# Kernel tuning notes

Measured on AMD Instinct MI355X. Metric: run time of the kernel, lower is better.

## Reference

```python
import jax, jax.numpy as jnp
import numpy as np

N = 4_194_304   # samples per polarization
L = 513         # impulse response taps


def setup_inputs() -> dict:
    key = jax.random.key(0)
    k1, k2, k3, k4 = jax.random.split(key, 4)
    tx_real = jax.random.normal(k1, (2, N), dtype=jnp.float32)
    tx_imag = jax.random.normal(k2, (2, N), dtype=jnp.float32)
    h_real = jax.random.normal(k3, (L,), dtype=jnp.float32)
    h_imag = jax.random.normal(k4, (L,), dtype=jnp.float32)
    return {"tx_real": tx_real, "tx_imag": tx_imag, "h_real": h_real, "h_imag": h_imag}


def reference(tx_real, tx_imag, h_real, h_imag):
    # Dual-pol complex baseband signal [2, N]; same taps h [L] applied to each pol.
    tx = tx_real + 1j * tx_imag          # complex64 [2, N]
    h = h_real + 1j * h_imag             # complex64 [L]
    n_out = tx.shape[-1] + h.shape[0] - 1  # 'full' convolution length
    # FFT-based full convolution, both polarizations batched in one FFT call
    # (mathematically identical to overlap-save convolution in 'full' mode).
    X = jnp.fft.fft(tx, n=n_out, axis=-1)   # [2, n_out]
    H = jnp.fft.fft(h, n=n_out)             # [n_out]
    y = jnp.fft.ifft(X * H[None, :], axis=-1)  # [2, n_out] complex
    # Return real/imag stacked so the output is a real array: [2, n_out, 2]
    return jnp.stack([y.real, y.imag], axis=-1)
```

## Files before the change

### kernel.cpp

```cpp
#include <hip/hip_runtime.h>
#include <hip/hip_bf16.h>


#define NSAMP 4194304
#define LTAPS 513
#define NOUT  (NSAMP + LTAPS - 1)

#define BLK       256
#define WAVE_OUT  1024
#define BLOCK_OUT 4096
#define HALO      512
#define XELEMS    (BLOCK_OUT + HALO + 16)
#define NB        34
#define HROWS     592
#define NBLK      ((NOUT + BLOCK_OUT - 1) / BLOCK_OUT)

typedef __attribute__((ext_vector_type(8)))  short short8;
typedef __attribute__((ext_vector_type(4)))  short short4v;
typedef __attribute__((ext_vector_type(4)))  int   int4v;
typedef __attribute__((ext_vector_type(16))) float float16v;

__device__ __forceinline__ int xswz(int e) { return e ^ (((e >> 6) & 7) << 3); }
#define XSZ 4624

__device__ __forceinline__ short f2b(float f) {
    __bf16 b = (__bf16)f;
    return __builtin_bit_cast(short, b);
}

__global__ __launch_bounds__(BLK)
void build_h(const float* __restrict__ hr, const float* __restrict__ hi,
             short* __restrict__ hh) {
    int R = blockIdx.x * BLK + threadIdx.x;
    if (R < HROWS) {
        short8 vr, vi;
        #pragma unroll
        for (int j = 0; j < 8; ++j) {
            int idx = R - 24 - j;
            bool ok = (idx >= 0) && (idx < LTAPS);
            vr[j] = f2b(ok ? hr[idx] : 0.0f);
            vi[j] = f2b(ok ? hi[idx] : 0.0f);
        }
        *(short8*)(hh + (size_t)(0 * HROWS + R) * 8) = vr;
        *(short8*)(hh + (size_t)(1 * HROWS + R) * 8) = vi;
    }
}

#define MFMA32(A, B, C) __builtin_amdgcn_mfma_f32_32x32x16_bf16((A), (B), (C), 0, 0, 0)

__device__ __forceinline__ short8 bneg8(short8 v) {
    int4v t = __builtin_bit_cast(int4v, v);
    t ^= (int4v){(int)0x80008000, (int)0x80008000, (int)0x80008000, (int)0x80008000};
    return __builtin_bit_cast(short8, t);
}

__global__ __launch_bounds__(BLK, 4)
void fir_mfma32w(const float* __restrict__ txr_all, const float* __restrict__ txi_all,
                 const short* __restrict__ hh, float2* __restrict__ out) {
    const int N0  = blockIdx.x * BLOCK_OUT;
    const int tid = threadIdx.x;

    __shared__ __align__(16) short xs[4][XSZ];

    #pragma unroll
    for (int p = 0; p < 2; ++p) {
        const float* __restrict__ xr_g = txr_all + (size_t)p * NSAMP;
        const float* __restrict__ xi_g = txi_all + (size_t)p * NSAMP;
        #pragma unroll
        for (int it = 0; it < 5; ++it) {
            int e = (tid + it * BLK) * 4;
            if (e < XELEMS) {
                int g = N0 - HALO + e;
                float r0, r1, r2, r3, i0, i1, i2, i3;
                if (g >= 0 && g + 3 < NSAMP) {
                    float4 fr = *(const float4*)(xr_g + g);
                    float4 fi = *(const float4*)(xi_g + g);
                    r0 = fr.x; r1 = fr.y; r2 = fr.z; r3 = fr.w;
                    i0 = fi.x; i1 = fi.y; i2 = fi.z; i3 = fi.w;
                } else {
                    int gc0 = min(max(g + 0, 0), NSAMP - 1);
                    int gc1 = min(max(g + 1, 0), NSAMP - 1);
                    int gc2 = min(max(g + 2, 0), NSAMP - 1);
                    int gc3 = min(max(g + 3, 0), NSAMP - 1);
                    r0 = (g + 0 >= 0 && g + 0 < NSAMP) ? xr_g[gc0] : 0.0f;
                    r1 = (g + 1 >= 0 && g + 1 < NSAMP) ? xr_g[gc1] : 0.0f;
                    r2 = (g + 2 >= 0 && g + 2 < NSAMP) ? xr_g[gc2] : 0.0f;
                    r3 = (g + 3 >= 0 && g + 3 < NSAMP) ? xr_g[gc3] : 0.0f;
                    i0 = (g + 0 >= 0 && g + 0 < NSAMP) ? xi_g[gc0] : 0.0f;
                    i1 = (g + 1 >= 0 && g + 1 < NSAMP) ? xi_g[gc1] : 0.0f;
                    i2 = (g + 2 >= 0 && g + 2 < NSAMP) ? xi_g[gc2] : 0.0f;
                    i3 = (g + 3 >= 0 && g + 3 < NSAMP) ? xi_g[gc3] : 0.0f;
                }
                int ls = xswz(e);
                short4v vr = { f2b(r0), f2b(r1), f2b(r2), f2b(r3) };
                short4v vi = { f2b(i0), f2b(i1), f2b(i2), f2b(i3) };
                *(short4v*)(&xs[2 * p + 0][ls]) = vr;
                *(short4v*)(&xs[2 * p + 1][ls]) = vi;
            }
        }
    }
    __syncthreads();

    const int lane  = tid & 63;
    const int wave  = tid >> 6;
    const int strip = wave;
    const int cc    = lane & 31;
    const int half  = lane >> 5;

    float16v zero = {0.f,0.f,0.f,0.f,0.f,0.f,0.f,0.f,0.f,0.f,0.f,0.f,0.f,0.f,0.f,0.f};
    float16v acc_re0 = zero, acc_im0 = zero, acc_re1 = zero, acc_im1 = zero;

    const int    ebase = HALO + strip * WAVE_OUT + 32 * cc + 8 * half + 16;
    const short* hpr   = hh + (size_t)(cc - 8 * half + 8) * 8;
    const short* xb    = &xs[0][0];

    int ls0 = xswz(ebase);
    short8 fxr0 = *(const short8*)(xb + ls0);
    short8 fxi0 = *(const short8*)(xb + XSZ + ls0);
    short8 fxr1 = *(const short8*)(xb + 2 * XSZ + ls0);
    short8 fxi1 = *(const short8*)(xb + 3 * XSZ + ls0);
    short8 fhr  = *(const short8*)(hpr);
    short8 fhi  = *(const short8*)(hpr + (size_t)HROWS * 8);

    #pragma unroll 2
    for (int b = 0; b < NB; ++b) {
        int en = ebase - 16 * (b + 1);
        en = en < 0 ? 0 : en;
        int lsn = xswz(en);
        short8 nxr0 = *(const short8*)(xb + lsn);
        short8 nxi0 = *(const short8*)(xb + XSZ + lsn);
        short8 nxr1 = *(const short8*)(xb + 2 * XSZ + lsn);
        short8 nxi1 = *(const short8*)(xb + 3 * XSZ + lsn);
        const short* hn = hpr + (size_t)(16 * (b + 1)) * 8;
        short8 nhr = *(const short8*)(hn);
        short8 nhi = *(const short8*)(hn + (size_t)HROWS * 8);

        short8 fnhi = bneg8(fhi);
        acc_re0 = MFMA32(fxr0, fhr,  acc_re0);
        acc_im0 = MFMA32(fxi0, fhr,  acc_im0);
        acc_re1 = MFMA32(fxr1, fhr,  acc_re1);
        acc_im1 = MFMA32(fxi1, fhr,  acc_im1);
        acc_re0 = MFMA32(fxi0, fnhi, acc_re0);
        acc_im0 = MFMA32(fxr0, fhi,  acc_im0);
        acc_re1 = MFMA32(fxi1, fnhi, acc_re1);
        acc_im1 = MFMA32(fxr1, fhi,  acc_im1);

        fxr0 = nxr0; fxi0 = nxi0; fxr1 = nxr1; fxi1 = nxi1;
        fhr  = nhr;  fhi  = nhi;
    }

    float2* __restrict__ op0 = out;
    float2* __restrict__ op1 = out + (size_t)NOUT;
    const int nw = N0 + strip * WAVE_OUT;
    #pragma unroll
    for (int v = 0; v < 16; ++v) {
        int row = (v & 3) + 8 * (v >> 2) + 4 * half;
        int n = nw + 32 * row + cc;
        if (n < NOUT) {
            op0[n] = make_float2(acc_re0[v], acc_im0[v]);
            op1[n] = make_float2(acc_re1[v], acc_im1[v]);
        }
    }
}

extern "C" void kernel_launch(void* const* d_in, const int* in_sizes, int n_in,
                              void* d_out, int out_size, void* d_ws, size_t ws_size,
                              hipStream_t stream) {
    const float* txr = (const float*)d_in[0];
    const float* txi = (const float*)d_in[1];
    const float* hr  = (const float*)d_in[2];
    const float* hi  = (const float*)d_in[3];
    float2* out = (float2*)d_out;
    short* hh = (short*)d_ws;

    build_h<<<dim3((HROWS + BLK - 1) / BLK), BLK, 0, stream>>>(hr, hi, hh);

    fir_mfma32w<<<dim3(NBLK), BLK, 0, stream>>>(txr, txi, hh, out);
}
```

Measured before the change: 140.7 us.

## Persistent double-buffered FIR kernel overlapping next tile loads with MFMA compute

Replaces the one-tile-per-block launch with a persistent grid of 256 blocks of 512 threads. Each block walks 8192-sample tiles, prefetching the next tile's inputs into registers while computing the current tile, then writing them to a second LDS buffer. Taps are copied into LDS once per block. Interior tiles skip the bounds-checked load path, and only edge tiles use it. The cost is higher register and LDS pressure, lower occupancy (2 blocks/CU), and only two tile iterations per block.

Result: no change. 141.8 us (+0.8%).

```diff
diff --git a/kernel.cpp b/kernel.cpp
--- a/kernel.cpp
+++ b/kernel.cpp
@@ -6,14 +6,17 @@
 #define LTAPS 513
 #define NOUT  (NSAMP + LTAPS - 1)
 
-#define BLK       256
+#define BLK       512
 #define WAVE_OUT  1024
-#define BLOCK_OUT 4096
+#define BLOCK_OUT 8192
 #define HALO      512
 #define XELEMS    (BLOCK_OUT + HALO + 16)
 #define NB        34
 #define HROWS     592
-#define NBLK      ((NOUT + BLOCK_OUT - 1) / BLOCK_OUT)
+#define GRID      256
+#define NT        513
+#define XEL_MINI  1552
+#define SITER     5
 
 typedef __attribute__((ext_vector_type(8)))  short short8;
 typedef __attribute__((ext_vector_type(4)))  short short4v;
@@ -21,7 +24,7 @@
 typedef __attribute__((ext_vector_type(16))) float float16v;
 
 __device__ __forceinline__ int xswz(int e) { return e ^ (((e >> 6) & 7) << 3); }
-#define XSZ 4624
+#define XSZ XELEMS
 
 __device__ __forceinline__ short f2b(float f) {
     __bf16 b = (__bf16)f;
@@ -54,112 +57,184 @@
     return __builtin_bit_cast(short8, t);
 }
 
-__global__ __launch_bounds__(BLK, 4)
-void fir_mfma32w(const float* __restrict__ txr_all, const float* __restrict__ txi_all,
-                 const short* __restrict__ hh, float2* __restrict__ out) {
-    const int N0  = blockIdx.x * BLOCK_OUT;
+__device__ __forceinline__ bool tile_edge(int t) { return (t == 0) || (t >= 511); }
+
+__global__ __launch_bounds__(BLK, 2)
+void fir_pipe(const float* __restrict__ txr_all, const float* __restrict__ txi_all,
+              const short* __restrict__ hh, float2* __restrict__ out) {
+    const int bid = blockIdx.x;
     const int tid = threadIdx.x;
 
-    __shared__ __align__(16) short xs[4][XSZ];
-
-    #pragma unroll
-    for (int p = 0; p < 2; ++p) {
-        const float* __restrict__ xr_g = txr_all + (size_t)p * NSAMP;
-        const float* __restrict__ xi_g = txi_all + (size_t)p * NSAMP;
-        #pragma unroll
-        for (int it = 0; it < 5; ++it) {
-            int e = (tid + it * BLK) * 4;
-            if (e < XELEMS) {
-                int g = N0 - HALO + e;
-                float r0, r1, r2, r3, i0, i1, i2, i3;
-                if (g >= 0 && g + 3 < NSAMP) {
-                    float4 fr = *(const float4*)(xr_g + g);
-                    float4 fi = *(const float4*)(xi_g + g);
-                    r0 = fr.x; r1 = fr.y; r2 = fr.z; r3 = fr.w;
-                    i0 = fi.x; i1 = fi.y; i2 = fi.z; i3 = fi.w;
-                } else {
-                    int gc0 = min(max(g + 0, 0), NSAMP - 1);
-                    int gc1 = min(max(g + 1, 0), NSAMP - 1);
-                    int gc2 = min(max(g + 2, 0), NSAMP - 1);
-                    int gc3 = min(max(g + 3, 0), NSAMP - 1);
-                    r0 = (g + 0 >= 0 && g + 0 < NSAMP) ? xr_g[gc0] : 0.0f;
-                    r1 = (g + 1 >= 0 && g + 1 < NSAMP) ? xr_g[gc1] : 0.0f;
-                    r2 = (g + 2 >= 0 && g + 2 < NSAMP) ? xr_g[gc2] : 0.0f;
-                    r3 = (g + 3 >= 0 && g + 3 < NSAMP) ? xr_g[gc3] : 0.0f;
-                    i0 = (g + 0 >= 0 && g + 0 < NSAMP) ? xi_g[gc0] : 0.0f;
-                    i1 = (g + 1 >= 0 && g + 1 < NSAMP) ? xi_g[gc1] : 0.0f;
-                    i2 = (g + 2 >= 0 && g + 2 < NSAMP) ? xi_g[gc2] : 0.0f;
-                    i3 = (g + 3 >= 0 && g + 3 < NSAMP) ? xi_g[gc3] : 0.0f;
+    __shared__ __align__(16) short xs[2][4][XSZ];
+    __shared__ __align__(16) short hl[2 * HROWS * 8];
+
+    {
+        const int4* src = (const int4*)hh;
+        int4* dst = (int4*)hl;
+        #pragma unroll
+        for (int it = 0; it < 3; ++it) {
+            int idx = tid + it * BLK;
+            if (idx < 2 * HROWS) dst[idx] = src[idx];
+        }
+    }
+
+    float4 fr[2][SITER], fi[2][SITER];
+
+    auto stage_load = [&](int t) {
+        if (tile_edge(t)) return;
+        const int N0 = t * BLOCK_OUT;
+        #pragma unroll
+        for (int p = 0; p < 2; ++p) {
+            const float* __restrict__ xr_g = txr_all + (size_t)p * NSAMP + (N0 - HALO);
+            const float* __restrict__ xi_g = txi_all + (size_t)p * NSAMP + (N0 - HALO);
+            #pragma unroll
+            for (int it = 0; it < SITER; ++it) {
+                int e = (tid + it * BLK) * 4;
+                if (e < XELEMS) {
+                    fr[p][it] = *(const float4*)(xr_g + e);
+                    fi[p][it] = *(const float4*)(xi_g + e);
                 }
-                int ls = xswz(e);
-                short4v vr = { f2b(r0), f2b(r1), f2b(r2), f2b(r3) };
-                short4v vi = { f2b(i0), f2b(i1), f2b(i2), f2b(i3) };
-                *(short4v*)(&xs[2 * p + 0][ls]) = vr;
-                *(short4v*)(&xs[2 * p + 1][ls]) = vi;
-            }
-        }
-    }
+            }
+        }
+    };
+
+    auto stage_write = [&](int t, int buf) {
+        if (!tile_edge(t)) {
+            #pragma unroll
+            for (int p = 0; p < 2; ++p) {
+                #pragma unroll
+                for (int it = 0; it < SITER; ++it) {
+                    int e = (tid + it * BLK) * 4;
+                    if (e < XELEMS) {
+                        int ls = xswz(e);
+                        float4 r = fr[p][it], i = fi[p][it];
+                        short4v vr = { f2b(r.x), f2b(r.y), f2b(r.z), f2b(r.w) };
+                        short4v vi = { f2b(i.x), f2b(i.y), f2b(i.z), f2b(i.w) };
+                        *(short4v*)(&xs[buf][2 * p + 0][ls]) = vr;
+                        *(short4v*)(&xs[buf][2 * p + 1][ls]) = vi;
+                    }
+                }
+            }
+        } else {
+            const int N0  = t * BLOCK_OUT;
+            const int xel = (t == NT - 1) ? XEL_MINI : XELEMS;
+            for (int p = 0; p < 2; ++p) {
+                const float* __restrict__ xr_g = txr_all + (size_t)p * NSAMP;
+                const float* __restrict__ xi_g = txi_all + (size_t)p * NSAMP;
+                for (int it = 0; it < SITER; ++it) {
+                    int e = (tid + it * BLK) * 4;
+                    if (e < xel) {
+                        int g = N0 - HALO + e;
+                        float r0, r1, r2, r3, i0, i1, i2, i3;
+                        if (g >= 0 && g + 3 < NSAMP) {
+                            float4 frv = *(const float4*)(xr_g + g);
+                            float4 fiv = *(const float4*)(xi_g + g);
+                            r0 = frv.x; r1 = frv.y; r2 = frv.z; r3 = frv.w;
+                            i0 = fiv.x; i1 = fiv.y; i2 = fiv.z; i3 = fiv.w;
+                        } else {
+                            int gc0 = min(max(g + 0, 0), NSAMP - 1);
+                            int gc1 = min(max(g + 1, 0), NSAMP - 1);
+                            int gc2 = min(max(g + 2, 0), NSAMP - 1);
+                            int gc3 = min(max(g + 3, 0), NSAMP - 1);
+                            r0 = (g + 0 >= 0 && g + 0 < NSAMP) ? xr_g[gc0] : 0.0f;
+                            r1 = (g + 1 >= 0 && g + 1 < NSAMP) ? xr_g[gc1] : 0.0f;
+                            r2 = (g + 2 >= 0 && g + 2 < NSAMP) ? xr_g[gc2] : 0.0f;
+                            r3 = (g + 3 >= 0 && g + 3 < NSAMP) ? xr_g[gc3] : 0.0f;
+                            i0 = (g + 0 >= 0 && g + 0 < NSAMP) ? xi_g[gc0] : 0.0f;
+                            i1 = (g + 1 >= 0 && g + 1 < NSAMP) ? xi_g[gc1] : 0.0f;
+                            i2 = (g + 2 >= 0 && g + 2 < NSAMP) ? xi_g[gc2] : 0.0f;
+                            i3 = (g + 3 >= 0 && g + 3 < NSAMP) ? xi_g[gc3] : 0.0f;
+                        }
+                        int ls = xswz(e);
+                        short4v vr = { f2b(r0), f2b(r1), f2b(r2), f2b(r3) };
+                        short4v vi = { f2b(i0), f2b(i1), f2b(i2), f2b(i3) };
+                        *(short4v*)(&xs[buf][2 * p + 0][ls]) = vr;
+                        *(short4v*)(&xs[buf][2 * p + 1][ls]) = vi;
+                    }
+                }
+            }
+        }
+    };
+
+    const int lane = tid & 63;
+    const int wave = tid >> 6;
+    const int cc   = lane & 31;
+    const int half = lane >> 5;
+    const short* hp0 = hl + (size_t)(cc - 8 * half + 8) * 8;
+
+    auto compute_store = [&](int t, int buf) {
+        const int N0 = t * BLOCK_OUT;
+        const int nw = N0 + wave * WAVE_OUT;
+        if (nw >= NOUT) return;
+
+        float16v zero = {0.f,0.f,0.f,0.f,0.f,0.f,0.f,0.f,0.f,0.f,0.f,0.f,0.f,0.f,0.f,0.f};
+        float16v acc_re0 = zero, acc_im0 = zero, acc_re1 = zero, acc_im1 = zero;
+
+        const int    ebase = HALO + wave * WAVE_OUT + 32 * cc + 8 * half + 16;
+        const short* xb    = &xs[buf][0][0];
+
+        int ls0 = xswz(ebase);
+        short8 fxr0 = *(const short8*)(xb + ls0);
+        short8 fxi0 = *(const short8*)(xb + XSZ + ls0);
+        short8 fxr1 = *(const short8*)(xb + 2 * XSZ + ls0);
+        short8 fxi1 = *(const short8*)(xb + 3 * XSZ + ls0);
+        short8 fhr  = *(const short8*)(hp0);
+        short8 fhi  = *(const short8*)(hp0 + (size_t)HROWS * 8);
+
+        #pragma unroll 2
+        for (int b = 0; b < NB; ++b) {
+            int en = ebase - 16 * (b + 1);
+            en = en < 0 ? 0 : en;
+            int lsn = xswz(en);
+            short8 nxr0 = *(const short8*)(xb + lsn);
+            short8 nxi0 = *(const short8*)(xb + XSZ + lsn);
+            short8 nxr1 = *(const short8*)(xb + 2 * XSZ + lsn);
+            short8 nxi1 = *(const short8*)(xb + 3 * XSZ + lsn);
+            const short* hn = hp0 + (size_t)(16 * (b + 1)) * 8;
+            short8 nhr = *(const short8*)(hn);
+            short8 nhi = *(const short8*)(hn + (size_t)HROWS * 8);
+
+            short8 fnhi = bneg8(fhi);
+            acc_re0 = MFMA32(fxr0, fhr,  acc_re0);
+            acc_im0 = MFMA32(fxi0, fhr,  acc_im0);
+            acc_re1 = MFMA32(fxr1, fhr,  acc_re1);
+            acc_im1 = MFMA32(fxi1, fhr,  acc_im1);
+            acc_re0 = MFMA32(fxi0, fnhi, acc_re0);
+            acc_im0 = MFMA32(fxr0, fhi,  acc_im0);
+            acc_re1 = MFMA32(fxi1, fnhi, acc_re1);
+            acc_im1 = MFMA32(fxr1, fhi,  acc_im1);
+
+            fxr0 = nxr0; fxi0 = nxi0; fxr1 = nxr1; fxi1 = nxi1;
+            fhr  = nhr;  fhi  = nhi;
+        }
+
+        float2* __restrict__ op0 = out;
+        float2* __restrict__ op1 = out + (size_t)NOUT;
+        #pragma unroll
+        for (int v = 0; v < 16; ++v) {
+            int row = (v & 3) + 8 * (v >> 2) + 4 * half;
+            int n = nw + 32 * row + cc;
+            if (n < NOUT) {
+                op0[n] = make_float2(acc_re0[v], acc_im0[v]);
+                op1[n] = make_float2(acc_re1[v], acc_im1[v]);
+            }
+        }
+    };
+
+    stage_load(bid);
+    stage_write(bid, 0);
     __syncthreads();
 
-    const int lane  = tid & 63;
-    const int wave  = tid >> 6;
-    const int strip = wave;
-    const int cc    = lane & 31;
-    const int half  = lane >> 5;
-
-    float16v zero = {0.f,0.f,0.f,0.f,0.f,0.f,0.f,0.f,0.f,0.f,0.f,0.f,0.f,0.f,0.f,0.f};
-    float16v acc_re0 = zero, acc_im0 = zero, acc_re1 = zero, acc_im1 = zero;
-
-    const int    ebase = HALO + strip * WAVE_OUT + 32 * cc + 8 * half + 16;
-    const short* hpr   = hh + (size_t)(cc - 8 * half + 8) * 8;
-    const short* xb    = &xs[0][0];
-
-    int ls0 = xswz(ebase);
-    short8 fxr0 = *(const short8*)(xb + ls0);
-    short8 fxi0 = *(const short8*)(xb + XSZ + ls0);
-    short8 fxr1 = *(const short8*)(xb + 2 * XSZ + ls0);
-    short8 fxi1 = *(const short8*)(xb + 3 * XSZ + ls0);
-    short8 fhr  = *(const short8*)(hpr);
-    short8 fhi  = *(const short8*)(hpr + (size_t)HROWS * 8);
-
-    #pragma unroll 2
-    for (int b = 0; b < NB; ++b) {
-        int en = ebase - 16 * (b + 1);
-        en = en < 0 ? 0 : en;
-        int lsn = xswz(en);
-        short8 nxr0 = *(const short8*)(xb + lsn);
-        short8 nxi0 = *(const short8*)(xb + XSZ + lsn);
-        short8 nxr1 = *(const short8*)(xb + 2 * XSZ + lsn);
-        short8 nxi1 = *(const short8*)(xb + 3 * XSZ + lsn);
-        const short* hn = hpr + (size_t)(16 * (b + 1)) * 8;
-        short8 nhr = *(const short8*)(hn);
-        short8 nhi = *(const short8*)(hn + (size_t)HROWS * 8);
-
-        short8 fnhi = bneg8(fhi);
-        acc_re0 = MFMA32(fxr0, fhr,  acc_re0);
-        acc_im0 = MFMA32(fxi0, fhr,  acc_im0);
-        acc_re1 = MFMA32(fxr1, fhr,  acc_re1);
-        acc_im1 = MFMA32(fxi1, fhr,  acc_im1);
-        acc_re0 = MFMA32(fxi0, fnhi, acc_re0);
-        acc_im0 = MFMA32(fxr0, fhi,  acc_im0);
-        acc_re1 = MFMA32(fxi1, fnhi, acc_re1);
-        acc_im1 = MFMA32(fxr1, fhi,  acc_im1);
-
-        fxr0 = nxr0; fxi0 = nxi0; fxr1 = nxr1; fxi1 = nxi1;
-        fhr  = nhr;  fhi  = nhi;
-    }
-
-    float2* __restrict__ op0 = out;
-    float2* __restrict__ op1 = out + (size_t)NOUT;
-    const int nw = N0 + strip * WAVE_OUT;
-    #pragma unroll
-    for (int v = 0; v < 16; ++v) {
-        int row = (v & 3) + 8 * (v >> 2) + 4 * half;
-        int n = nw + 32 * row + cc;
-        if (n < NOUT) {
-            op0[n] = make_float2(acc_re0[v], acc_im0[v]);
-            op1[n] = make_float2(acc_re1[v], acc_im1[v]);
-        }
+    int cur = 0;
+    for (int t = bid; t < NT; t += GRID) {
+        int tn = t + GRID;
+        if (tn < NT) stage_load(tn);
+        compute_store(t, cur);
+        if (tn < NT) {
+            stage_write(tn, cur ^ 1);
+            __syncthreads();
+        }
+        cur ^= 1;
     }
 }
 
@@ -175,5 +250,5 @@
 
     build_h<<<dim3((HROWS + BLK - 1) / BLK), BLK, 0, stream>>>(hr, hi, hh);
 
-    fir_mfma32w<<<dim3(NBLK), BLK, 0, stream>>>(txr, txi, hh, out);
-}
+    fir_pipe<<<dim3(GRID), BLK, 0, stream>>>(txr, txi, hh, out);
+}
```

## Use fixed 512-block grid with two tiles per block and staggered load/compute phases

Applied to the files above, without the earlier changes.

Replaces the one-tile-per-block launch (1025 blocks) with a fixed grid of 512 blocks, each processing tiles bid and bid+512 using double-buffered LDS. Half of the blocks stage both tiles up front and the other half alternate stage/compute, so memory-bound and MFMA-bound phases are offset across the GPU. A fast path without bounds checks is added for interior tiles, and the last block handles the leftover tile. LDS per block doubles and occupancy bound drops to 2, which can reduce latency hiding.

New measurement: 147.0 us. +4.5%, slower.

```diff
diff --git a/kernel.cpp b/kernel.cpp
--- a/kernel.cpp
+++ b/kernel.cpp
@@ -13,7 +13,9 @@
 #define XELEMS    (BLOCK_OUT + HALO + 16)
 #define NB        34
 #define HROWS     592
-#define NBLK      ((NOUT + BLOCK_OUT - 1) / BLOCK_OUT)
+#define GRID      512
+#define RUNT      1024
+#define SITER     5
 
 typedef __attribute__((ext_vector_type(8)))  short short8;
 typedef __attribute__((ext_vector_type(4)))  short short4v;
@@ -21,7 +23,7 @@
 typedef __attribute__((ext_vector_type(16))) float float16v;
 
 __device__ __forceinline__ int xswz(int e) { return e ^ (((e >> 6) & 7) << 3); }
-#define XSZ 4624
+#define XSZ XELEMS
 
 __device__ __forceinline__ short f2b(float f) {
     __bf16 b = (__bf16)f;
@@ -54,73 +56,97 @@
     return __builtin_bit_cast(short8, t);
 }
 
-__global__ __launch_bounds__(BLK, 4)
-void fir_mfma32w(const float* __restrict__ txr_all, const float* __restrict__ txi_all,
-                 const short* __restrict__ hh, float2* __restrict__ out) {
-    const int N0  = blockIdx.x * BLOCK_OUT;
-    const int tid = threadIdx.x;
-
-    __shared__ __align__(16) short xs[4][XSZ];
-
-    #pragma unroll
-    for (int p = 0; p < 2; ++p) {
-        const float* __restrict__ xr_g = txr_all + (size_t)p * NSAMP;
-        const float* __restrict__ xi_g = txi_all + (size_t)p * NSAMP;
+#define BAR()  do {                                         \
+        asm volatile("s_waitcnt lgkmcnt(0)" ::: "memory");  \
+        __builtin_amdgcn_s_barrier();                       \
+        __builtin_amdgcn_sched_barrier(0);                  \
+    } while (0)
+
+__device__ __forceinline__ void stage_tile(
+        const float* __restrict__ txr_all, const float* __restrict__ txi_all,
+        short (*__restrict__ xsb)[XSZ], int t, int tid) {
+    const int N0 = t * BLOCK_OUT;
+    const bool edge = (t == 0) || (t >= 1023);
+    if (!edge) {
+        const long gb = (long)N0 - HALO;
         #pragma unroll
-        for (int it = 0; it < 5; ++it) {
-            int e = (tid + it * BLK) * 4;
-            if (e < XELEMS) {
-                int g = N0 - HALO + e;
-                float r0, r1, r2, r3, i0, i1, i2, i3;
-                if (g >= 0 && g + 3 < NSAMP) {
-                    float4 fr = *(const float4*)(xr_g + g);
-                    float4 fi = *(const float4*)(xi_g + g);
-                    r0 = fr.x; r1 = fr.y; r2 = fr.z; r3 = fr.w;
-                    i0 = fi.x; i1 = fi.y; i2 = fi.z; i3 = fi.w;
-                } else {
-                    int gc0 = min(max(g + 0, 0), NSAMP - 1);
-                    int gc1 = min(max(g + 1, 0), NSAMP - 1);
-                    int gc2 = min(max(g + 2, 0), NSAMP - 1);
-                    int gc3 = min(max(g + 3, 0), NSAMP - 1);
-                    r0 = (g + 0 >= 0 && g + 0 < NSAMP) ? xr_g[gc0] : 0.0f;
-                    r1 = (g + 1 >= 0 && g + 1 < NSAMP) ? xr_g[gc1] : 0.0f;
-                    r2 = (g + 2 >= 0 && g + 2 < NSAMP) ? xr_g[gc2] : 0.0f;
-                    r3 = (g + 3 >= 0 && g + 3 < NSAMP) ? xr_g[gc3] : 0.0f;
-                    i0 = (g + 0 >= 0 && g + 0 < NSAMP) ? xi_g[gc0] : 0.0f;
-                    i1 = (g + 1 >= 0 && g + 1 < NSAMP) ? xi_g[gc1] : 0.0f;
-                    i2 = (g + 2 >= 0 && g + 2 < NSAMP) ? xi_g[gc2] : 0.0f;
-                    i3 = (g + 3 >= 0 && g + 3 < NSAMP) ? xi_g[gc3] : 0.0f;
+        for (int p = 0; p < 2; ++p) {
+            const float* __restrict__ xr_g = txr_all + (size_t)p * NSAMP + gb;
+            const float* __restrict__ xi_g = txi_all + (size_t)p * NSAMP + gb;
+            #pragma unroll
+            for (int it = 0; it < SITER; ++it) {
+                int e = (tid + it * BLK) * 4;
+                if (e < XELEMS) {
+                    float4 r = *(const float4*)(xr_g + e);
+                    float4 i = *(const float4*)(xi_g + e);
+                    int ls = xswz(e);
+                    short4v vr = { f2b(r.x), f2b(r.y), f2b(r.z), f2b(r.w) };
+                    short4v vi = { f2b(i.x), f2b(i.y), f2b(i.z), f2b(i.w) };
+                    *(short4v*)(&xsb[2 * p + 0][ls]) = vr;
+                    *(short4v*)(&xsb[2 * p + 1][ls]) = vi;
                 }
-                int ls = xswz(e);
-                short4v vr = { f2b(r0), f2b(r1), f2b(r2), f2b(r3) };
-                short4v vi = { f2b(i0), f2b(i1), f2b(i2), f2b(i3) };
-                *(short4v*)(&xs[2 * p + 0][ls]) = vr;
-                *(short4v*)(&xs[2 * p + 1][ls]) = vi;
             }
         }
-    }
-    __syncthreads();
-
-    const int lane  = tid & 63;
-    const int wave  = tid >> 6;
-    const int strip = wave;
-    const int cc    = lane & 31;
-    const int half  = lane >> 5;
+    } else {
+        for (int p = 0; p < 2; ++p) {
+            const float* __restrict__ xr_g = txr_all + (size_t)p * NSAMP;
+            const float* __restrict__ xi_g = txi_all + (size_t)p * NSAMP;
+            for (int it = 0; it < SITER; ++it) {
+                int e = (tid + it * BLK) * 4;
+                if (e < XELEMS) {
+                    int g = N0 - HALO + e;
+                    float r0, r1, r2, r3, i0, i1, i2, i3;
+                    if (g >= 0 && g + 3 < NSAMP) {
+                        float4 fr = *(const float4*)(xr_g + g);
+                        float4 fi = *(const float4*)(xi_g + g);
+                        r0 = fr.x; r1 = fr.y; r2 = fr.z; r3 = fr.w;
+                        i0 = fi.x; i1 = fi.y; i2 = fi.z; i3 = fi.w;
+                    } else {
+                        int gc0 = min(max(g + 0, 0), NSAMP - 1);
+                        int gc1 = min(max(g + 1, 0), NSAMP - 1);
+                        int gc2 = min(max(g + 2, 0), NSAMP - 1);
+                        int gc3 = min(max(g + 3, 0), NSAMP - 1);
+                        r0 = (g + 0 >= 0 && g + 0 < NSAMP) ? xr_g[gc0] : 0.0f;
+                        r1 = (g + 1 >= 0 && g + 1 < NSAMP) ? xr_g[gc1] : 0.0f;
+                        r2 = (g + 2 >= 0 && g + 2 < NSAMP) ? xr_g[gc2] : 0.0f;
+                        r3 = (g + 3 >= 0 && g + 3 < NSAMP) ? xr_g[gc3] : 0.0f;
+                        i0 = (g + 0 >= 0 && g + 0 < NSAMP) ? xi_g[gc0] : 0.0f;
+                        i1 = (g + 1 >= 0 && g + 1 < NSAMP) ? xi_g[gc1] : 0.0f;
+                        i2 = (g + 2 >= 0 && g + 2 < NSAMP) ? xi_g[gc2] : 0.0f;
+                        i3 = (g + 3 >= 0 && g + 3 < NSAMP) ? xi_g[gc3] : 0.0f;
+                    }
+                    int ls = xswz(e);
+                    short4v vr = { f2b(r0), f2b(r1), f2b(r2), f2b(r3) };
+                    short4v vi = { f2b(i0), f2b(i1), f2b(i2), f2b(i3) };
+                    *(short4v*)(&xsb[2 * p + 0][ls]) = vr;
+                    *(short4v*)(&xsb[2 * p + 1][ls]) = vi;
+                }
+            }
+        }
+    }
+}
+
+__device__ __forceinline__ void compute_tile(
+        const short* __restrict__ hh, float2* __restrict__ out,
+        const short* __restrict__ xb, int t, int lane, int wave) {
+    const int nw = t * BLOCK_OUT + wave * WAVE_OUT;
+    if (nw >= NOUT) return;
+
+    const int cc   = lane & 31;
+    const int half = lane >> 5;
+    const short* hp0  = hh + (size_t)(cc - 8 * half + 8) * 8;
+    const int   ebase = HALO + wave * WAVE_OUT + 32 * cc + 8 * half + 16;
 
     float16v zero = {0.f,0.f,0.f,0.f,0.f,0.f,0.f,0.f,0.f,0.f,0.f,0.f,0.f,0.f,0.f,0.f};
     float16v acc_re0 = zero, acc_im0 = zero, acc_re1 = zero, acc_im1 = zero;
-
-    const int    ebase = HALO + strip * WAVE_OUT + 32 * cc + 8 * half + 16;
-    const short* hpr   = hh + (size_t)(cc - 8 * half + 8) * 8;
-    const short* xb    = &xs[0][0];
 
     int ls0 = xswz(ebase);
     short8 fxr0 = *(const short8*)(xb + ls0);
     short8 fxi0 = *(const short8*)(xb + XSZ + ls0);
     short8 fxr1 = *(const short8*)(xb + 2 * XSZ + ls0);
     short8 fxi1 = *(const short8*)(xb + 3 * XSZ + ls0);
-    short8 fhr  = *(const short8*)(hpr);
-    short8 fhi  = *(const short8*)(hpr + (size_t)HROWS * 8);
+    short8 fhr  = *(const short8*)(hp0);
+    short8 fhi  = *(const short8*)(hp0 + (size_t)HROWS * 8);
 
     #pragma unroll 2
     for (int b = 0; b < NB; ++b) {
@@ -131,7 +157,7 @@
         short8 nxi0 = *(const short8*)(xb + XSZ + lsn);
         short8 nxr1 = *(const short8*)(xb + 2 * XSZ + lsn);
         short8 nxi1 = *(const short8*)(xb + 3 * XSZ + lsn);
-        const short* hn = hpr + (size_t)(16 * (b + 1)) * 8;
+        const short* hn = hp0 + (size_t)(16 * (b + 1)) * 8;
         short8 nhr = *(const short8*)(hn);
         short8 nhi = *(const short8*)(hn + (size_t)HROWS * 8);
 
@@ -151,7 +177,6 @@
 
     float2* __restrict__ op0 = out;
     float2* __restrict__ op1 = out + (size_t)NOUT;
-    const int nw = N0 + strip * WAVE_OUT;
     #pragma unroll
     for (int v = 0; v < 16; ++v) {
         int row = (v & 3) + 8 * (v >> 2) + 4 * half;
@@ -160,6 +185,43 @@
             op0[n] = make_float2(acc_re0[v], acc_im0[v]);
             op1[n] = make_float2(acc_re1[v], acc_im1[v]);
         }
+    }
+}
+
+__global__ __launch_bounds__(BLK, 2)
+void fir_stag(const float* __restrict__ txr_all, const float* __restrict__ txi_all,
+              const short* __restrict__ hh, float2* __restrict__ out) {
+    const int bid  = blockIdx.x;
+    const int tid  = threadIdx.x;
+    const int lane = tid & 63;
+    const int wave = tid >> 6;
+
+    __shared__ __align__(16) short xs[2][4][XSZ];
+
+    const int t0 = bid;
+    const int t1 = bid + GRID;
+    const bool stagger = (bid >> 8) & 1;
+
+    if (stagger) {
+        stage_tile(txr_all, txi_all, xs[0], t0, tid);
+        stage_tile(txr_all, txi_all, xs[1], t1, tid);
+        BAR();
+        compute_tile(hh, out, &xs[0][0][0], t0, lane, wave);
+        compute_tile(hh, out, &xs[1][0][0], t1, lane, wave);
+    } else {
+        stage_tile(txr_all, txi_all, xs[0], t0, tid);
+        BAR();
+        compute_tile(hh, out, &xs[0][0][0], t0, lane, wave);
+        stage_tile(txr_all, txi_all, xs[1], t1, tid);
+        BAR();
+        compute_tile(hh, out, &xs[1][0][0], t1, lane, wave);
+    }
+
+    if (bid == GRID - 1) {
+        BAR();
+        stage_tile(txr_all, txi_all, xs[0], RUNT, tid);
+        BAR();
+        compute_tile(hh, out, &xs[0][0][0], RUNT, lane, wave);
     }
 }
 
@@ -175,5 +237,5 @@
 
     build_h<<<dim3((HROWS + BLK - 1) / BLK), BLK, 0, stream>>>(hr, hi, hh);
 
-    fir_mfma32w<<<dim3(NBLK), BLK, 0, stream>>>(txr, txi, hh, out);
-}
+    fir_stag<<<dim3(GRID), BLK, 0, stream>>>(txr, txi, hh, out);
+}
```

## Pre-convert input to padded bf16 planes and run FIR directly from global memory

Applied to the files above, without the earlier changes.

Adds a pre-pass that converts the fp32 input into zero-padded bf16 planes in workspace. The FIR kernel then reads its MFMA operands straight from global/L2 with no bounds checks or per-block LDS staging, and keeps the taps in LDS instead. This removes the halo reload, the conversion and the block-wide sync from the main kernel. In exchange it adds an extra kernel launch and a full write-then-read of bf16 planes, and operand loads become global rather than LDS. The original kernel is kept as a fallback when the workspace is too small.

Measured after the change: 168.8 us. 1.2x slower.

```diff
diff --git a/kernel.cpp b/kernel.cpp
--- a/kernel.cpp
+++ b/kernel.cpp
@@ -6,22 +6,20 @@
 #define LTAPS 513
 #define NOUT  (NSAMP + LTAPS - 1)
 
-#define BLK       256
-#define WAVE_OUT  1024
-#define BLOCK_OUT 4096
-#define HALO      512
-#define XELEMS    (BLOCK_OUT + HALO + 16)
-#define NB        34
-#define HROWS     592
-#define NBLK      ((NOUT + BLOCK_OUT - 1) / BLOCK_OUT)
+#define NB     34
+#define HROWS  592
+#define PAD    1024
+#define PLN    (PAD + NSAMP + PAD)
+#define NSTRIP 4097
+#define BLK    256
+
+#define PLANE_OFF  32768
+#define WS_NEED    ((size_t)PLANE_OFF + 4ull * PLN * 2ull)
 
 typedef __attribute__((ext_vector_type(8)))  short short8;
 typedef __attribute__((ext_vector_type(4)))  short short4v;
 typedef __attribute__((ext_vector_type(4)))  int   int4v;
 typedef __attribute__((ext_vector_type(16))) float float16v;
-
-__device__ __forceinline__ int xswz(int e) { return e ^ (((e >> 6) & 7) << 3); }
-#define XSZ 4624
 
 __device__ __forceinline__ short f2b(float f) {
     __bf16 b = (__bf16)f;
@@ -46,6 +44,33 @@
     }
 }
 
+#define UNITS_PER_PLANE (PLN / 8)
+#define CVT_BLOCKS      ((4 * UNITS_PER_PLANE) / BLK)
+
+__global__ __launch_bounds__(BLK)
+void cvt_pad(const float* __restrict__ txr, const float* __restrict__ txi,
+             short* __restrict__ planes) {
+    int u = blockIdx.x * BLK + threadIdx.x;
+    int p = u / UNITS_PER_PLANE;
+    int q = u - p * UNITS_PER_PLANE;
+    const float* __restrict__ src = ((p & 1) ? txi : txr) + (size_t)(p >> 1) * NSAMP;
+    int e0 = q * 8 - PAD;
+    short8 v;
+    if (e0 >= 0 && e0 + 8 <= NSAMP) {
+        float4 a = *(const float4*)(src + e0);
+        float4 b = *(const float4*)(src + e0 + 4);
+        v[0] = f2b(a.x); v[1] = f2b(a.y); v[2] = f2b(a.z); v[3] = f2b(a.w);
+        v[4] = f2b(b.x); v[5] = f2b(b.y); v[6] = f2b(b.z); v[7] = f2b(b.w);
+    } else {
+        #pragma unroll
+        for (int j = 0; j < 8; ++j) {
+            int g = e0 + j;
+            v[j] = (g >= 0 && g < NSAMP) ? f2b(src[g]) : (short)0;
+        }
+    }
+    *(short8*)(planes + (size_t)p * PLN + (size_t)q * 8) = v;
+}
+
 #define MFMA32(A, B, C) __builtin_amdgcn_mfma_f32_32x32x16_bf16((A), (B), (C), 0, 0, 0)
 
 __device__ __forceinline__ short8 bneg8(short8 v) {
@@ -54,13 +79,102 @@
     return __builtin_bit_cast(short8, t);
 }
 
+__global__ __launch_bounds__(BLK, 3)
+void fir_direct(const short* __restrict__ planes, const short* __restrict__ hh,
+                float2* __restrict__ out) {
+    __shared__ __align__(16) short hl[2 * HROWS * 8];
+
+    const int tid = threadIdx.x;
+    {
+        const int4* src = (const int4*)hh;
+        int4* dst = (int4*)hl;
+        #pragma unroll
+        for (int it = 0; it < 10; ++it) {
+            int idx = tid + it * BLK;
+            if (idx < (2 * HROWS * 8 * 2) / 16) dst[idx] = src[idx];
+        }
+    }
+    __syncthreads();
+
+    const int lane = tid & 63;
+    const int wave = tid >> 6;
+    const int cc   = lane & 31;
+    const int half = lane >> 5;
+
+    const int s = blockIdx.x * 4 + wave;
+    if (s >= NSTRIP) return;
+    const int nw = s * 1024;
+
+    const short* __restrict__ x0 = planes;
+    const short* __restrict__ x1 = planes + (size_t)PLN;
+    const short* __restrict__ x2 = planes + (size_t)2 * PLN;
+    const short* __restrict__ x3 = planes + (size_t)3 * PLN;
+
+    const int    e0  = PAD + nw + 32 * cc + 8 * half + 16;
+    const short* hp0 = hl + (size_t)(cc - 8 * half + 8) * 8;
+
+    float16v zero = {0.f,0.f,0.f,0.f,0.f,0.f,0.f,0.f,0.f,0.f,0.f,0.f,0.f,0.f,0.f,0.f};
+    float16v acc_re0 = zero, acc_im0 = zero, acc_re1 = zero, acc_im1 = zero;
+
+    short8 fxr0 = *(const short8*)(x0 + e0);
+    short8 fxi0 = *(const short8*)(x1 + e0);
+    short8 fxr1 = *(const short8*)(x2 + e0);
+    short8 fxi1 = *(const short8*)(x3 + e0);
+    short8 fhr  = *(const short8*)(hp0);
+    short8 fhi  = *(const short8*)(hp0 + (size_t)HROWS * 8);
+
+    #pragma unroll 2
+    for (int b = 0; b < NB; ++b) {
+        const int en = e0 - 16 * (b + 1);
+        short8 nxr0 = *(const short8*)(x0 + en);
+        short8 nxi0 = *(const short8*)(x1 + en);
+        short8 nxr1 = *(const short8*)(x2 + en);
+        short8 nxi1 = *(const short8*)(x3 + en);
+        const short* hn = hp0 + (size_t)(16 * (b + 1)) * 8;
+        short8 nhr = *(const short8*)(hn);
+        short8 nhi = *(const short8*)(hn + (size_t)HROWS * 8);
+
+        short8 fnhi = bneg8(fhi);
+        acc_re0 = MFMA32(fxr0, fhr,  acc_re0);
+        acc_im0 = MFMA32(fxi0, fhr,  acc_im0);
+        acc_re1 = MFMA32(fxr1, fhr,  acc_re1);
+        acc_im1 = MFMA32(fxi1, fhr,  acc_im1);
+        acc_re0 = MFMA32(fxi0, fnhi, acc_re0);
+        acc_im0 = MFMA32(fxr0, fhi,  acc_im0);
+        acc_re1 = MFMA32(fxi1, fnhi, acc_re1);
+        acc_im1 = MFMA32(fxr1, fhi,  acc_im1);
+
+        fxr0 = nxr0; fxi0 = nxi0; fxr1 = nxr1; fxi1 = nxi1;
+        fhr  = nhr;  fhi  = nhi;
+    }
+
+    float2* __restrict__ op0 = out;
+    float2* __restrict__ op1 = out + (size_t)NOUT;
+    #pragma unroll
+    for (int v = 0; v < 16; ++v) {
+        int row = (v & 3) + 8 * (v >> 2) + 4 * half;
+        int n = nw + 32 * row + cc;
+        if (n < NOUT) {
+            op0[n] = make_float2(acc_re0[v], acc_im0[v]);
+            op1[n] = make_float2(acc_re1[v], acc_im1[v]);
+        }
+    }
+}
+
+#define F_BLOCK_OUT 4096
+#define F_HALO      512
+#define F_XELEMS    (F_BLOCK_OUT + F_HALO + 16)
+#define F_XSZ       F_XELEMS
+#define F_NBLK      ((NOUT + F_BLOCK_OUT - 1) / F_BLOCK_OUT)
+
+__device__ __forceinline__ int f_xswz(int e) { return e ^ (((e >> 6) & 7) << 3); }
+
 __global__ __launch_bounds__(BLK, 4)
-void fir_mfma32w(const float* __restrict__ txr_all, const float* __restrict__ txi_all,
-                 const short* __restrict__ hh, float2* __restrict__ out) {
-    const int N0  = blockIdx.x * BLOCK_OUT;
+void fir_fb(const float* __restrict__ txr_all, const float* __restrict__ txi_all,
+            const short* __restrict__ hh, float2* __restrict__ out) {
+    const int N0  = blockIdx.x * F_BLOCK_OUT;
     const int tid = threadIdx.x;
-
-    __shared__ __align__(16) short xs[4][XSZ];
+    __shared__ __align__(16) short xs[4][F_XSZ];
 
     #pragma unroll
     for (int p = 0; p < 2; ++p) {
@@ -69,8 +183,8 @@
         #pragma unroll
         for (int it = 0; it < 5; ++it) {
             int e = (tid + it * BLK) * 4;
-            if (e < XELEMS) {
-                int g = N0 - HALO + e;
+            if (e < F_XELEMS) {
+                int g = N0 - F_HALO + e;
                 float r0, r1, r2, r3, i0, i1, i2, i3;
                 if (g >= 0 && g + 3 < NSAMP) {
                     float4 fr = *(const float4*)(xr_g + g);
@@ -91,7 +205,7 @@
                     i2 = (g + 2 >= 0 && g + 2 < NSAMP) ? xi_g[gc2] : 0.0f;
                     i3 = (g + 3 >= 0 && g + 3 < NSAMP) ? xi_g[gc3] : 0.0f;
                 }
-                int ls = xswz(e);
+                int ls = f_xswz(e);
                 short4v vr = { f2b(r0), f2b(r1), f2b(r2), f2b(r3) };
                 short4v vi = { f2b(i0), f2b(i1), f2b(i2), f2b(i3) };
                 *(short4v*)(&xs[2 * p + 0][ls]) = vr;
@@ -101,24 +215,23 @@
     }
     __syncthreads();
 
-    const int lane  = tid & 63;
-    const int wave  = tid >> 6;
-    const int strip = wave;
-    const int cc    = lane & 31;
-    const int half  = lane >> 5;
+    const int lane = tid & 63;
+    const int wave = tid >> 6;
+    const int cc   = lane & 31;
+    const int half = lane >> 5;
 
     float16v zero = {0.f,0.f,0.f,0.f,0.f,0.f,0.f,0.f,0.f,0.f,0.f,0.f,0.f,0.f,0.f,0.f};
     float16v acc_re0 = zero, acc_im0 = zero, acc_re1 = zero, acc_im1 = zero;
 
-    const int    ebase = HALO + strip * WAVE_OUT + 32 * cc + 8 * half + 16;
+    const int    ebase = F_HALO + wave * 1024 + 32 * cc + 8 * half + 16;
     const short* hpr   = hh + (size_t)(cc - 8 * half + 8) * 8;
     const short* xb    = &xs[0][0];
 
-    int ls0 = xswz(ebase);
+    int ls0 = f_xswz(ebase);
     short8 fxr0 = *(const short8*)(xb + ls0);
-    short8 fxi0 = *(const short8*)(xb + XSZ + ls0);
-    short8 fxr1 = *(const short8*)(xb + 2 * XSZ + ls0);
-    short8 fxi1 = *(const short8*)(xb + 3 * XSZ + ls0);
+    short8 fxi0 = *(const short8*)(xb + F_XSZ + ls0);
+    short8 fxr1 = *(const short8*)(xb + 2 * F_XSZ + ls0);
+    short8 fxi1 = *(const short8*)(xb + 3 * F_XSZ + ls0);
     short8 fhr  = *(const short8*)(hpr);
     short8 fhi  = *(const short8*)(hpr + (size_t)HROWS * 8);
 
@@ -126,11 +239,11 @@
     for (int b = 0; b < NB; ++b) {
         int en = ebase - 16 * (b + 1);
         en = en < 0 ? 0 : en;
-        int lsn = xswz(en);
+        int lsn = f_xswz(en);
         short8 nxr0 = *(const short8*)(xb + lsn);
-        short8 nxi0 = *(const short8*)(xb + XSZ + lsn);
-        short8 nxr1 = *(const short8*)(xb + 2 * XSZ + lsn);
-        short8 nxi1 = *(const short8*)(xb + 3 * XSZ + lsn);
+        short8 nxi0 = *(const short8*)(xb + F_XSZ + lsn);
+        short8 nxr1 = *(const short8*)(xb + 2 * F_XSZ + lsn);
+        short8 nxi1 = *(const short8*)(xb + 3 * F_XSZ + lsn);
         const short* hn = hpr + (size_t)(16 * (b + 1)) * 8;
         short8 nhr = *(const short8*)(hn);
         short8 nhi = *(const short8*)(hn + (size_t)HROWS * 8);
@@ -151,7 +264,7 @@
 
     float2* __restrict__ op0 = out;
     float2* __restrict__ op1 = out + (size_t)NOUT;
-    const int nw = N0 + strip * WAVE_OUT;
+    const int nw = N0 + wave * 1024;
     #pragma unroll
     for (int v = 0; v < 16; ++v) {
         int row = (v & 3) + 8 * (v >> 2) + 4 * half;
@@ -175,5 +288,11 @@
 
     build_h<<<dim3((HROWS + BLK - 1) / BLK), BLK, 0, stream>>>(hr, hi, hh);
 
-    fir_mfma32w<<<dim3(NBLK), BLK, 0, stream>>>(txr, txi, hh, out);
-}
+    if (ws_size >= WS_NEED) {
+        short* planes = (short*)((char*)d_ws + PLANE_OFF);
+        cvt_pad<<<dim3(CVT_BLOCKS), BLK, 0, stream>>>(txr, txi, planes);
+        fir_direct<<<dim3((NSTRIP + 3) / 4), BLK, 0, stream>>>(planes, hh, out);
+    } else {
+        fir_fb<<<dim3(F_NBLK), BLK, 0, stream>>>(txr, txi, hh, out);
+    }
+}
```
